# Optimization experiments

Measured on AMD Instinct MI355X. Metric: run time of the kernel, lower is better.

## Reference

```python
import jax, jax.numpy as jnp
import numpy as np

N, D_IN, D_HID, D_OUT, E = 50000, 256, 512, 256, 1000000

def setup_inputs() -> dict:
    key = jax.random.key(0)
    ks = jax.random.split(key, 8)
    x = jax.random.normal(ks[0], (N, D_IN), dtype=jnp.float32)
    edge_index = jax.random.randint(ks[1], (2, E), 0, N, dtype=jnp.int64)
    edge_weight = jax.random.uniform(ks[2], (E,), dtype=jnp.float32)
    # xavier-uniform linear weights, zero biases (as in reset_parameter)
    lim1 = float(np.sqrt(6.0 / (D_IN + D_HID)))
    W1 = jax.random.uniform(ks[3], (D_HID, D_IN), minval=-lim1, maxval=lim1, dtype=jnp.float32)
    b1 = jnp.zeros((D_HID,), jnp.float32)
    lim2 = float(np.sqrt(6.0 / (D_HID + D_OUT)))
    W2 = jax.random.uniform(ks[4], (D_OUT, D_HID), minval=-lim2, maxval=lim2, dtype=jnp.float32)
    b2 = jnp.zeros((D_OUT,), jnp.float32)
    return {"x": x, "edge_index": edge_index, "edge_weight": edge_weight,
            "W1": W1, "b1": b1, "W2": W2, "b2": b2}

def reference(x, edge_index, edge_weight, W1, b1, W2, b2):
    n = x.shape[0]
    loop = jnp.arange(n, dtype=edge_index.dtype)
    # gcn_norm: add self-loops (weight 1), symmetric normalization
    row = jnp.concatenate([edge_index[0], loop])   # source j
    col = jnp.concatenate([edge_index[1], loop])   # target i
    w = jnp.concatenate([edge_weight, jnp.ones((n,), x.dtype)])
    deg = jax.ops.segment_sum(w, col, num_segments=n)
    dinv = jnp.where(deg > 0, jax.lax.rsqrt(deg), 0.0)
    norm = dinv[row] * w * dinv[col]               # [E+N]
    # K=1 propagation: out[i] = sum_j norm_ij * x[j]
    agg = jax.ops.segment_sum(x[row] * norm[:, None], col, num_segments=n)  # [N, D_IN]
    h = jax.nn.relu(agg @ W1.T + b1)               # SGConv.lin + relu (dropout=eval -> identity)
    logits = h @ W2.T + b2
    return (logits, h)
```

## Files before the change

### kernel.cpp

```cpp
#include <hip/hip_runtime.h>

#define D_IN 256
#define D_HID 512
#define D_OUT 256

__global__ __launch_bounds__(256) void init_nodes(float* __restrict__ deg,
                                                  int* __restrict__ cnt, int N) {
    int i = blockIdx.x * 256 + threadIdx.x;
    if (i < N) { deg[i] = 1.0f; cnt[i] = 0; }
}

__global__ __launch_bounds__(256) void edge_deg(const int* __restrict__ ei,
                                                const float* __restrict__ ew,
                                                float* __restrict__ deg,
                                                int* __restrict__ cnt, int E) {
    int e = blockIdx.x * 256 + threadIdx.x;
    if (e < E) {
        int c = ei[E + e];
        atomicAdd(&deg[c], ew[e]);
        atomicAdd(&cnt[c], 1);
    }
}

__global__ __launch_bounds__(256) void make_dinv(float* __restrict__ deg, int N) {
    int i = blockIdx.x * 256 + threadIdx.x;
    if (i < N) deg[i] = rsqrtf(deg[i]);
}

__global__ __launch_bounds__(1024) void scan_excl(const int* __restrict__ cnt,
                                                  int* __restrict__ offs, int N) {
    __shared__ int wsum[16];
    int t = threadIdx.x;
    const int CH = (N + 1023) / 1024;
    int base = t * CH;
    int s = 0;
    for (int j = 0; j < CH; ++j) {
        int idx = base + j;
        if (idx < N) s += cnt[idx];
    }
    int lane = t & 63;
    int incl = s;
#pragma unroll
    for (int off = 1; off < 64; off <<= 1) {
        int v = __shfl_up(incl, off, 64);
        if (lane >= off) incl += v;
    }
    int wid = t >> 6;
    if (lane == 63) wsum[wid] = incl;
    __syncthreads();
    if (t < 16) {
        int v = wsum[t];
#pragma unroll
        for (int off = 1; off < 16; off <<= 1) {
            int u = __shfl_up(v, off, 64);
            if (t >= off) v += u;
        }
        wsum[t] = v;
    }
    __syncthreads();
    int waveoff = (wid == 0) ? 0 : wsum[wid - 1];
    int run = waveoff + incl - s;
    for (int j = 0; j < CH; ++j) {
        int idx = base + j;
        if (idx < N) { offs[idx] = run; run += cnt[idx]; }
    }
}

__global__ __launch_bounds__(256) void fill_edges(const int* __restrict__ ei,
                                                  const float* __restrict__ ew,
                                                  const float* __restrict__ dinv,
                                                  int* __restrict__ offs,
                                                  int2* __restrict__ epk, int E) {
    int e = blockIdx.x * 256 + threadIdx.x;
    if (e < E) {
        int r = ei[e];
        int c = ei[E + e];
        float nm = dinv[r] * ew[e] * dinv[c];
        int pos = atomicAdd(&offs[c], 1);
        int2 p; p.x = r; p.y = __float_as_int(nm);
        epk[pos] = p;
    }
}

__global__ __launch_bounds__(64) void gather_agg(const float* __restrict__ x,
                                                 const int2* __restrict__ epk,
                                                 const int* __restrict__ offs,
                                                 const float* __restrict__ dinv,
                                                 float* __restrict__ agg, int N) {
    int i = blockIdx.x;
    int lane = threadIdx.x;
    int start = (i == 0) ? 0 : offs[i - 1];
    int end = offs[i];
    float di = dinv[i];
    float sw = di * di;
    float4 acc = *(const float4*)(x + (size_t)i * D_IN + lane * 4);
    acc.x *= sw; acc.y *= sw; acc.z *= sw; acc.w *= sw;
#pragma unroll 2
    for (int e = start; e < end; ++e) {
        int2 p = epk[e];
        float nm = __int_as_float(p.y);
        const float4 v = *(const float4*)(x + (size_t)p.x * D_IN + lane * 4);
        acc.x = fmaf(nm, v.x, acc.x);
        acc.y = fmaf(nm, v.y, acc.y);
        acc.z = fmaf(nm, v.z, acc.z);
        acc.w = fmaf(nm, v.w, acc.w);
    }
    *(float4*)(agg + (size_t)i * D_IN + lane * 4) = acc;
}

template <bool RELU>
__global__ __launch_bounds__(256) void gemm_nt(const float* __restrict__ A,
                                               const float* __restrict__ B,
                                               const float* __restrict__ bias,
                                               float* __restrict__ C,
                                               int M, int K, int NO) {
    const int BK = 32;
    __shared__ float As[BK][132];
    __shared__ float Bs[BK][132];
    int t = threadIdx.x;
    int m0 = blockIdx.y * 128;
    int n0 = blockIdx.x * 128;
    int tx = t & 15, ty = t >> 4;
    int ra = t >> 1;
    int kq = (t & 1) * 16;

    float acc[8][8];
#pragma unroll
    for (int i = 0; i < 8; ++i)
#pragma unroll
        for (int j = 0; j < 8; ++j) acc[i][j] = 0.0f;

    int mrow = m0 + ra; if (mrow > M - 1) mrow = M - 1;
    const float* Aptr = A + (size_t)mrow * K + kq;
    const float* Bptr = B + (size_t)(n0 + ra) * K + kq;

    for (int k0 = 0; k0 < K; k0 += BK) {
#pragma unroll
        for (int j = 0; j < 4; ++j) {
            int kk = kq + j * 4;
            float4 va = *(const float4*)(Aptr + k0 + j * 4);
            As[kk + 0][ra] = va.x; As[kk + 1][ra] = va.y;
            As[kk + 2][ra] = va.z; As[kk + 3][ra] = va.w;
            float4 vb = *(const float4*)(Bptr + k0 + j * 4);
            Bs[kk + 0][ra] = vb.x; Bs[kk + 1][ra] = vb.y;
            Bs[kk + 2][ra] = vb.z; Bs[kk + 3][ra] = vb.w;
        }
        __syncthreads();
#pragma unroll
        for (int k = 0; k < BK; ++k) {
            float a[8], b[8];
            *(float4*)&a[0] = *(const float4*)&As[k][ty * 8];
            *(float4*)&a[4] = *(const float4*)&As[k][ty * 8 + 4];
            *(float4*)&b[0] = *(const float4*)&Bs[k][tx * 8];
            *(float4*)&b[4] = *(const float4*)&Bs[k][tx * 8 + 4];
#pragma unroll
            for (int i = 0; i < 8; ++i)
#pragma unroll
                for (int j = 0; j < 8; ++j)
                    acc[i][j] = fmaf(a[i], b[j], acc[i][j]);
        }
        __syncthreads();
    }

    float bv[8];
    *(float4*)&bv[0] = *(const float4*)(bias + n0 + tx * 8);
    *(float4*)&bv[4] = *(const float4*)(bias + n0 + tx * 8 + 4);
#pragma unroll
    for (int i = 0; i < 8; ++i) {
        int m = m0 + ty * 8 + i;
        if (m < M) {
            float out[8];
#pragma unroll
            for (int j = 0; j < 8; ++j) {
                float v = acc[i][j] + bv[j];
                out[j] = RELU ? fmaxf(v, 0.0f) : v;
            }
            *(float4*)(C + (size_t)m * NO + n0 + tx * 8) = *(float4*)&out[0];
            *(float4*)(C + (size_t)m * NO + n0 + tx * 8 + 4) = *(float4*)&out[4];
        }
    }
}

extern "C" void kernel_launch(void* const* d_in, const int* in_sizes, int n_in,
                              void* d_out, int out_size, void* d_ws, size_t ws_size,
                              hipStream_t stream) {
    const float* x  = (const float*)d_in[0];
    const int*   ei = (const int*)d_in[1];
    const float* ew = (const float*)d_in[2];
    const float* W1 = (const float*)d_in[3];
    const float* b1 = (const float*)d_in[4];
    const float* W2 = (const float*)d_in[5];
    const float* b2 = (const float*)d_in[6];

    const int N = in_sizes[0] / D_IN;
    const int E = in_sizes[2];

    char* ws = (char*)d_ws;
    size_t off = 0;
    auto take = [&](size_t bytes) -> char* {
        char* p = ws + off;
        off += (bytes + 255) & ~(size_t)255;
        return p;
    };
    float* deg  = (float*)take((size_t)N * 4);
    int*   cnt  = (int*)take((size_t)N * 4);
    int*   offs = (int*)take((size_t)N * 4);
    int2*  epk  = (int2*)take((size_t)E * 8);

    float* agg    = (float*)d_out;
    float* h      = (float*)d_out + (size_t)N * D_IN;
    float* logits = (float*)d_out;

    int nb = (N + 255) / 256;
    int eb = (E + 255) / 256;

    init_nodes<<<nb, 256, 0, stream>>>(deg, cnt, N);
    edge_deg<<<eb, 256, 0, stream>>>(ei, ew, deg, cnt, E);
    make_dinv<<<nb, 256, 0, stream>>>(deg, N);
    scan_excl<<<1, 1024, 0, stream>>>(cnt, offs, N);
    fill_edges<<<eb, 256, 0, stream>>>(ei, ew, deg, offs, epk, E);
    gather_agg<<<N, 64, 0, stream>>>(x, epk, offs, deg, agg, N);

    dim3 g1(D_HID / 128, (N + 127) / 128);
    gemm_nt<true><<<g1, 256, 0, stream>>>(agg, W1, b1, h, N, D_IN, D_HID);
    dim3 g2(D_OUT / 128, (N + 127) / 128);
    gemm_nt<false><<<g2, 256, 0, stream>>>(h, W2, b2, logits, N, D_HID, D_OUT);
}
```

Before: 879.3 us.

## Replace FP32 SIMT GEMMs with split-bf16 MFMA GEMMs using async LDS loads

Both dense layers now run on MFMA bf16 matrix instructions, using a three-term hi/lo bf16 split to approximate fp32 accuracy. The aggregation kernel writes the split bf16 halves of agg directly, and small kernels pre-split the weights. The second GEMM converts h from fp32 inside its load stage. B tiles, and A tiles for the first GEMM, are loaded with global_load_lds async copies. This trades three MFMAs per product and extra split kernels for removing the slow FP32 FMA inner loop, at a small precision risk.

```diff
diff --git a/kernel.cpp b/kernel.cpp
--- a/kernel.cpp
+++ b/kernel.cpp
@@ -1,8 +1,25 @@
 #include <hip/hip_runtime.h>
+
+typedef __bf16 bf16;
+typedef __attribute__((ext_vector_type(8))) __bf16 bf16x8;
+typedef __attribute__((ext_vector_type(4))) __bf16 bf16x4;
+typedef __attribute__((ext_vector_type(4))) float f32x4;
 
 #define D_IN 256
 #define D_HID 512
 #define D_OUT 256
+
+__device__ inline void async_copy16(void* lds_dst, const void* g_src) {
+    __builtin_amdgcn_global_load_lds(
+        (const __attribute__((address_space(1))) unsigned int*)g_src,
+        (__attribute__((address_space(3))) unsigned int*)lds_dst, 16, 0, 0);
+}
+
+struct bfpair { bf16 h, l; };
+__device__ inline bfpair split2(float f) {
+    bf16 hh = (bf16)f;
+    return { hh, (bf16)(f - (float)hh) };
+}
 
 __global__ __launch_bounds__(256) void init_nodes(float* __restrict__ deg,
                                                   int* __restrict__ cnt, int N) {
@@ -86,7 +103,8 @@
                                                  const int2* __restrict__ epk,
                                                  const int* __restrict__ offs,
                                                  const float* __restrict__ dinv,
-                                                 float* __restrict__ agg, int N) {
+                                                 bf16* __restrict__ Ahi,
+                                                 bf16* __restrict__ Alo, int N) {
     int i = blockIdx.x;
     int lane = threadIdx.x;
     int start = (i == 0) ? 0 : offs[i - 1];
@@ -105,78 +123,168 @@
         acc.z = fmaf(nm, v.z, acc.z);
         acc.w = fmaf(nm, v.w, acc.w);
     }
-    *(float4*)(agg + (size_t)i * D_IN + lane * 4) = acc;
-}
-
-template <bool RELU>
-__global__ __launch_bounds__(256) void gemm_nt(const float* __restrict__ A,
-                                               const float* __restrict__ B,
-                                               const float* __restrict__ bias,
-                                               float* __restrict__ C,
-                                               int M, int K, int NO) {
-    const int BK = 32;
-    __shared__ float As[BK][132];
-    __shared__ float Bs[BK][132];
-    int t = threadIdx.x;
-    int m0 = blockIdx.y * 128;
-    int n0 = blockIdx.x * 128;
-    int tx = t & 15, ty = t >> 4;
-    int ra = t >> 1;
-    int kq = (t & 1) * 16;
-
-    float acc[8][8];
-#pragma unroll
-    for (int i = 0; i < 8; ++i)
-#pragma unroll
-        for (int j = 0; j < 8; ++j) acc[i][j] = 0.0f;
-
-    int mrow = m0 + ra; if (mrow > M - 1) mrow = M - 1;
-    const float* Aptr = A + (size_t)mrow * K + kq;
-    const float* Bptr = B + (size_t)(n0 + ra) * K + kq;
-
-    for (int k0 = 0; k0 < K; k0 += BK) {
-#pragma unroll
-        for (int j = 0; j < 4; ++j) {
-            int kk = kq + j * 4;
-            float4 va = *(const float4*)(Aptr + k0 + j * 4);
-            As[kk + 0][ra] = va.x; As[kk + 1][ra] = va.y;
-            As[kk + 2][ra] = va.z; As[kk + 3][ra] = va.w;
-            float4 vb = *(const float4*)(Bptr + k0 + j * 4);
-            Bs[kk + 0][ra] = vb.x; Bs[kk + 1][ra] = vb.y;
-            Bs[kk + 2][ra] = vb.z; Bs[kk + 3][ra] = vb.w;
+    bf16x4 hv, lv;
+    bfpair p0 = split2(acc.x); hv[0] = p0.h; lv[0] = p0.l;
+    bfpair p1 = split2(acc.y); hv[1] = p1.h; lv[1] = p1.l;
+    bfpair p2 = split2(acc.z); hv[2] = p2.h; lv[2] = p2.l;
+    bfpair p3 = split2(acc.w); hv[3] = p3.h; lv[3] = p3.l;
+    size_t o = (size_t)i * D_IN + lane * 4;
+    *(bf16x4*)(Ahi + o) = hv;
+    *(bf16x4*)(Alo + o) = lv;
+}
+
+__global__ __launch_bounds__(256) void split_pair(const float* __restrict__ src,
+                                                  bf16* __restrict__ hi,
+                                                  bf16* __restrict__ lo, int n) {
+    int i = (blockIdx.x * 256 + threadIdx.x) * 4;
+    if (i < n) {
+        float4 v = *(const float4*)(src + i);
+        bf16x4 hv, lv;
+        bfpair p0 = split2(v.x); hv[0] = p0.h; lv[0] = p0.l;
+        bfpair p1 = split2(v.y); hv[1] = p1.h; lv[1] = p1.l;
+        bfpair p2 = split2(v.z); hv[2] = p2.h; lv[2] = p2.l;
+        bfpair p3 = split2(v.w); hv[3] = p3.h; lv[3] = p3.l;
+        *(bf16x4*)(hi + i) = hv;
+        *(bf16x4*)(lo + i) = lv;
+    }
+}
+
+template <bool RELU, bool CVT_A>
+__global__ __launch_bounds__(256) void gemm_mfma(
+    const bf16* __restrict__ Ahi, const bf16* __restrict__ Alo,
+    const float* __restrict__ Af32,
+    const bf16* __restrict__ Bhi, const bf16* __restrict__ Blo,
+    const float* __restrict__ bias, float* __restrict__ C,
+    int M, int K, int NO) {
+    __shared__ bf16 sAhi[4 * 128 * 8];
+    __shared__ bf16 sAlo[4 * 128 * 8];
+    __shared__ bf16 sBhi[4 * 128 * 8];
+    __shared__ bf16 sBlo[4 * 128 * 8];
+
+    const int t = threadIdx.x;
+    const int l = t & 63;
+    const int w = t >> 6;
+    const int m0 = blockIdx.y * 128;
+    const int n0 = blockIdx.x * 128;
+    const int wm = w >> 1, wn = w & 1;
+
+    size_t boff[2];
+    int dchunk[2];
+    size_t aoff[2];
+#pragma unroll
+    for (int j = 0; j < 2; ++j) {
+        int c = j * 256 + w * 64 + l;
+        int kg = c >> 7, row = c & 127;
+        boff[j] = (size_t)(n0 + row) * K + kg * 8;
+        dchunk[j] = (j * 256 + w * 64) * 8;
+        int rg = m0 + row; if (rg > M - 1) rg = M - 1;
+        aoff[j] = (size_t)rg * K + kg * 8;
+    }
+    const int rowA = t >> 1;
+    const int khA = (t & 1) * 16;
+    const int kgA = (t & 1) * 2;
+    const float* pA = nullptr;
+    if (CVT_A) {
+        int rg = m0 + rowA; if (rg > M - 1) rg = M - 1;
+        pA = Af32 + (size_t)rg * K + khA;
+    }
+
+    f32x4 acc[4][4];
+#pragma unroll
+    for (int mi = 0; mi < 4; ++mi)
+#pragma unroll
+        for (int ni = 0; ni < 4; ++ni) acc[mi][ni] = (f32x4){0.f, 0.f, 0.f, 0.f};
+
+    const int fl = l & 15;
+    const int fk = l >> 4;
+    const int abase = (fk * 128 + wm * 64 + fl) * 8;
+    const int bbase = (fk * 128 + wn * 64 + fl) * 8;
+
+    for (int k0 = 0; k0 < K; k0 += 32) {
+        bf16x8 h0, h1, l0v, l1v;
+        if (CVT_A) {
+            float4 va0 = *(const float4*)(pA + k0);
+            float4 va1 = *(const float4*)(pA + k0 + 4);
+            float4 va2 = *(const float4*)(pA + k0 + 8);
+            float4 va3 = *(const float4*)(pA + k0 + 12);
+            bfpair q;
+            q = split2(va0.x); h0[0] = q.h; l0v[0] = q.l;
+            q = split2(va0.y); h0[1] = q.h; l0v[1] = q.l;
+            q = split2(va0.z); h0[2] = q.h; l0v[2] = q.l;
+            q = split2(va0.w); h0[3] = q.h; l0v[3] = q.l;
+            q = split2(va1.x); h0[4] = q.h; l0v[4] = q.l;
+            q = split2(va1.y); h0[5] = q.h; l0v[5] = q.l;
+            q = split2(va1.z); h0[6] = q.h; l0v[6] = q.l;
+            q = split2(va1.w); h0[7] = q.h; l0v[7] = q.l;
+            q = split2(va2.x); h1[0] = q.h; l1v[0] = q.l;
+            q = split2(va2.y); h1[1] = q.h; l1v[1] = q.l;
+            q = split2(va2.z); h1[2] = q.h; l1v[2] = q.l;
+            q = split2(va2.w); h1[3] = q.h; l1v[3] = q.l;
+            q = split2(va3.x); h1[4] = q.h; l1v[4] = q.l;
+            q = split2(va3.y); h1[5] = q.h; l1v[5] = q.l;
+            q = split2(va3.z); h1[6] = q.h; l1v[6] = q.l;
+            q = split2(va3.w); h1[7] = q.h; l1v[7] = q.l;
         }
         __syncthreads();
 #pragma unroll
-        for (int k = 0; k < BK; ++k) {
-            float a[8], b[8];
-            *(float4*)&a[0] = *(const float4*)&As[k][ty * 8];
-            *(float4*)&a[4] = *(const float4*)&As[k][ty * 8 + 4];
-            *(float4*)&b[0] = *(const float4*)&Bs[k][tx * 8];
-            *(float4*)&b[4] = *(const float4*)&Bs[k][tx * 8 + 4];
-#pragma unroll
-            for (int i = 0; i < 8; ++i)
-#pragma unroll
-                for (int j = 0; j < 8; ++j)
-                    acc[i][j] = fmaf(a[i], b[j], acc[i][j]);
+        for (int j = 0; j < 2; ++j) {
+            async_copy16(sBhi + dchunk[j], Bhi + boff[j] + k0);
+            async_copy16(sBlo + dchunk[j], Blo + boff[j] + k0);
+            if (!CVT_A) {
+                async_copy16(sAhi + dchunk[j], Ahi + aoff[j] + k0);
+                async_copy16(sAlo + dchunk[j], Alo + aoff[j] + k0);
+            }
+        }
+        if (CVT_A) {
+            *(bf16x8*)(sAhi + (kgA * 128 + rowA) * 8) = h0;
+            *(bf16x8*)(sAhi + ((kgA + 1) * 128 + rowA) * 8) = h1;
+            *(bf16x8*)(sAlo + (kgA * 128 + rowA) * 8) = l0v;
+            *(bf16x8*)(sAlo + ((kgA + 1) * 128 + rowA) * 8) = l1v;
         }
         __syncthreads();
-    }
-
-    float bv[8];
-    *(float4*)&bv[0] = *(const float4*)(bias + n0 + tx * 8);
-    *(float4*)&bv[4] = *(const float4*)(bias + n0 + tx * 8 + 4);
-#pragma unroll
-    for (int i = 0; i < 8; ++i) {
-        int m = m0 + ty * 8 + i;
-        if (m < M) {
-            float out[8];
-#pragma unroll
-            for (int j = 0; j < 8; ++j) {
-                float v = acc[i][j] + bv[j];
-                out[j] = RELU ? fmaxf(v, 0.0f) : v;
+
+        bf16x8 ah[4], al[4], bh[4], bl[4];
+#pragma unroll
+        for (int mi = 0; mi < 4; ++mi) {
+            ah[mi] = *(const bf16x8*)(sAhi + abase + mi * 16 * 8);
+            al[mi] = *(const bf16x8*)(sAlo + abase + mi * 16 * 8);
+        }
+#pragma unroll
+        for (int ni = 0; ni < 4; ++ni) {
+            bh[ni] = *(const bf16x8*)(sBhi + bbase + ni * 16 * 8);
+            bl[ni] = *(const bf16x8*)(sBlo + bbase + ni * 16 * 8);
+        }
+#pragma unroll
+        for (int mi = 0; mi < 4; ++mi)
+#pragma unroll
+            for (int ni = 0; ni < 4; ++ni) {
+                acc[mi][ni] = __builtin_amdgcn_mfma_f32_16x16x32_bf16(
+                    ah[mi], bh[ni], acc[mi][ni], 0, 0, 0);
+                acc[mi][ni] = __builtin_amdgcn_mfma_f32_16x16x32_bf16(
+                    ah[mi], bl[ni], acc[mi][ni], 0, 0, 0);
+                acc[mi][ni] = __builtin_amdgcn_mfma_f32_16x16x32_bf16(
+                    al[mi], bh[ni], acc[mi][ni], 0, 0, 0);
             }
-            *(float4*)(C + (size_t)m * NO + n0 + tx * 8) = *(float4*)&out[0];
-            *(float4*)(C + (size_t)m * NO + n0 + tx * 8 + 4) = *(float4*)&out[4];
+    }
+
+    const int colb = n0 + wn * 64 + fl;
+    const int rowb = m0 + wm * 64 + fk * 4;
+    float bv[4];
+#pragma unroll
+    for (int ni = 0; ni < 4; ++ni) bv[ni] = bias[colb + ni * 16];
+#pragma unroll
+    for (int mi = 0; mi < 4; ++mi) {
+#pragma unroll
+        for (int r = 0; r < 4; ++r) {
+            int row = rowb + mi * 16 + r;
+            if (row < M) {
+#pragma unroll
+                for (int ni = 0; ni < 4; ++ni) {
+                    float v = acc[mi][ni][r] + bv[ni];
+                    if (RELU) v = fmaxf(v, 0.f);
+                    C[(size_t)row * NO + colb + ni * 16] = v;
+                }
+            }
         }
     }
 }
@@ -202,12 +310,17 @@
         off += (bytes + 255) & ~(size_t)255;
         return p;
     };
-    float* deg  = (float*)take((size_t)N * 4);
-    int*   cnt  = (int*)take((size_t)N * 4);
-    int*   offs = (int*)take((size_t)N * 4);
-    int2*  epk  = (int2*)take((size_t)E * 8);
-
-    float* agg    = (float*)d_out;
+    float* deg   = (float*)take((size_t)N * 4);
+    int*   cnt   = (int*)take((size_t)N * 4);
+    int*   offs  = (int*)take((size_t)N * 4);
+    int2*  epk   = (int2*)take((size_t)E * 8);
+    bf16*  W1hi  = (bf16*)take((size_t)D_HID * D_IN * 2);
+    bf16*  W1lo  = (bf16*)take((size_t)D_HID * D_IN * 2);
+    bf16*  W2hi  = (bf16*)take((size_t)D_OUT * D_HID * 2);
+    bf16*  W2lo  = (bf16*)take((size_t)D_OUT * D_HID * 2);
+
+    bf16*  Ahi    = (bf16*)d_out;
+    bf16*  Alo    = Ahi + (size_t)N * D_IN;
     float* h      = (float*)d_out + (size_t)N * D_IN;
     float* logits = (float*)d_out;
 
@@ -219,10 +332,17 @@
     make_dinv<<<nb, 256, 0, stream>>>(deg, N);
     scan_excl<<<1, 1024, 0, stream>>>(cnt, offs, N);
     fill_edges<<<eb, 256, 0, stream>>>(ei, ew, deg, offs, epk, E);
-    gather_agg<<<N, 64, 0, stream>>>(x, epk, offs, deg, agg, N);
+    gather_agg<<<N, 64, 0, stream>>>(x, epk, offs, deg, Ahi, Alo, N);
+
+    split_pair<<<(D_HID * D_IN) / 1024, 256, 0, stream>>>(W1, W1hi, W1lo, D_HID * D_IN);
+    split_pair<<<(D_OUT * D_HID) / 1024, 256, 0, stream>>>(W2, W2hi, W2lo, D_OUT * D_HID);
 
     dim3 g1(D_HID / 128, (N + 127) / 128);
-    gemm_nt<true><<<g1, 256, 0, stream>>>(agg, W1, b1, h, N, D_IN, D_HID);
+    gemm_mfma<true, false><<<g1, 256, 0, stream>>>(Ahi, Alo, nullptr,
+                                                   W1hi, W1lo, b1, h,
+                                                   N, D_IN, D_HID);
     dim3 g2(D_OUT / 128, (N + 127) / 128);
-    gemm_nt<false><<<g2, 256, 0, stream>>>(h, W2, b2, logits, N, D_HID, D_OUT);
-}
+    gemm_mfma<false, true><<<g2, 256, 0, stream>>>(nullptr, nullptr, h,
+                                                   W2hi, W2lo, b2, logits,
+                                                   N, D_HID, D_OUT);
+}
```

Result: faster. 707.3 us (-19.6%).
